# Optimization experiments

Hardware: AMD Instinct MI355X
Metric: run time of the kernel (lower is better)

Reference implementation:

```python
import jax, jax.numpy as jnp
import numpy as np

B, S, E, H = 2, 4096, 512, 8
DK = E // H


def setup_inputs() -> dict:
    k = jax.random.key(0)
    ks = jax.random.split(k, 11)
    sc = 0.02
    return {
        "query": jax.random.normal(ks[0], (B, S, E), jnp.float32),
        "key_in": jax.random.normal(ks[1], (B, S, E), jnp.float32),
        "value": jax.random.normal(ks[2], (B, S, E), jnp.float32),
        "Wq": jax.random.normal(ks[3], (E, E), jnp.float32) * sc,
        "bq": jax.random.normal(ks[4], (E,), jnp.float32) * sc,
        "Wk": jax.random.normal(ks[5], (E, E), jnp.float32) * sc,
        "bk": jax.random.normal(ks[6], (E,), jnp.float32) * sc,
        "Wv": jax.random.normal(ks[7], (E, E), jnp.float32) * sc,
        "bv": jax.random.normal(ks[8], (E,), jnp.float32) * sc,
        "Wo": jax.random.normal(ks[9], (E, E), jnp.float32) * sc,
        "bo": jax.random.normal(ks[10], (E,), jnp.float32) * sc,
    }


def reference(query, key_in, value, Wq, bq, Wk, bk, Wv, bv, Wo, bo):
    b, s, _ = query.shape
    # Linear projections
    q = query @ Wq + bq
    k = key_in @ Wk + bk
    v = value @ Wv + bv
    # [b, s, H, dk] -> [b, H, s, dk]
    q = q.reshape(b, s, H, DK).transpose(0, 2, 1, 3)
    k = k.reshape(b, s, H, DK).transpose(0, 2, 1, 3)
    v = v.reshape(b, s, H, DK).transpose(0, 2, 1, 3)
    # NOTE: source bug — softmax over UNSCALED scores (1/sqrt scaling in the
    # original is applied to a dead variable after softmax). Reproduce faithfully.
    scores = jnp.einsum("bhqd,bhkd->bhqk", q, k)  # [b,H,s,s] — O(N^2) materialized
    weights = jax.nn.softmax(scores.astype(jnp.float32), axis=-1)
    attn = jnp.einsum("bhqk,bhkd->bhqd", weights, v)
    # [b,H,s,dk] -> [b,s,E]
    concat = attn.transpose(0, 2, 1, 3).reshape(b, s, E)
    return concat @ Wo + bo
```

## Files before the change

kernel.cpp:

```cpp
#include <hip/hip_runtime.h>
#include <hip/hip_bf16.h>

#define B_  2
#define S_  4096
#define E_  512
#define H_  8
#define DK_ 64
#define M_  8192

typedef float f32x4  __attribute__((ext_vector_type(4)));
typedef float f32x16 __attribute__((ext_vector_type(16)));
typedef short s16x8  __attribute__((ext_vector_type(8)));
typedef short s16x4  __attribute__((ext_vector_type(4)));

static __device__ __forceinline__ short f2bf(float x) {
  __hip_bfloat16 h = __float2bfloat16(x);
  return __builtin_bit_cast(short, h);
}

static __device__ __forceinline__ f32x4 mfma32(s16x8 a, s16x8 b, f32x4 c) {
  return __builtin_amdgcn_mfma_f32_16x16x32_bf16(a, b, c, 0, 0, 0);
}

static __device__ __forceinline__ f32x16 mfma3232(s16x8 a, s16x8 b, f32x16 c) {
  return __builtin_amdgcn_mfma_f32_32x32x16_bf16(a, b, c, 0, 0, 0);
}

static __device__ __forceinline__ void gload_lds16(const void* g, void* l) {
  __builtin_amdgcn_global_load_lds(
      (const __attribute__((address_space(1))) unsigned int*)g,
      (__attribute__((address_space(3))) unsigned int*)l, 16, 0, 0);
}

static __device__ __forceinline__ int swz(int row, int colByte) {
  return row * 128 + (colByte ^ ((row & 7) << 4));
}

__global__ __launch_bounds__(256) void conv_bf16(const float* __restrict__ in,
                                                 short* __restrict__ out, int n4) {
  int i = blockIdx.x * 256 + threadIdx.x;
  if (i < n4) {
    float4 v = *((const float4*)in + i);
    s16x4 o;
    o[0] = f2bf(v.x); o[1] = f2bf(v.y); o[2] = f2bf(v.z); o[3] = f2bf(v.w);
    *((s16x4*)out + i) = o;
  }
}

__global__ __launch_bounds__(256) void conv_wT(const float* __restrict__ W,
                                               short* __restrict__ Wt) {
  int idx = blockIdx.x * 256 + threadIdx.x;
  int j = idx >> 9, k = idx & 511;
  Wt[idx] = f2bf(W[(size_t)k * E_ + j]);
}

static __device__ __forceinline__ void gemm_core_512(
    const short* __restrict__ A, const short* __restrict__ Bt,
    short* As, short* Bs, int tm, int tn, f32x4 acc[4][4]) {
  const int tid = threadIdx.x;
  const int wave = tid >> 6, lane = tid & 63;
  const int wm = (wave >> 1) * 64, wn = (wave & 1) * 64;
  const int c = lane & 15, g = lane >> 4;
  for (int kk = 0; kk < 512; kk += 64) {
#pragma unroll
    for (int i = 0; i < 4; ++i) {
      int ob = wave * 4096 + i * 1024 + lane * 16;
      int row = ob >> 7;
      int col = (ob & 127) >> 1;
      gload_lds16(A + (size_t)(tm + row) * 512 + kk + col,
                  (char*)As + wave * 4096 + i * 1024);
      gload_lds16(Bt + (size_t)(tn + row) * 512 + kk + col,
                  (char*)Bs + wave * 4096 + i * 1024);
    }
    __syncthreads();
#pragma unroll
    for (int s = 0; s < 2; ++s) {
      s16x8 af[4], bfr[4];
#pragma unroll
      for (int i = 0; i < 4; ++i)
        af[i] = *(const s16x8*)&As[(wm + i * 16 + c) * 64 + s * 32 + g * 8];
#pragma unroll
      for (int j = 0; j < 4; ++j)
        bfr[j] = *(const s16x8*)&Bs[(wn + j * 16 + c) * 64 + s * 32 + g * 8];
#pragma unroll
      for (int i = 0; i < 4; ++i)
#pragma unroll
        for (int j = 0; j < 4; ++j)
          acc[i][j] = mfma32(af[i], bfr[j], acc[i][j]);
    }
    __syncthreads();
  }
}

__global__ __launch_bounds__(256) void gemm_qkv(
    const short* __restrict__ Xq, const short* __restrict__ Xk,
    const short* __restrict__ Xv, const short* __restrict__ Wt,
    const float* __restrict__ bq, const float* __restrict__ bk,
    const float* __restrict__ bv,
    short* __restrict__ Qo, short* __restrict__ Ko, short* __restrict__ Vto) {
  __shared__ __align__(16) short As[128 * 64];
  __shared__ __align__(16) short Bs[128 * 64];
  const int z = blockIdx.z;
  const short* A = (z == 0) ? Xq : ((z == 1) ? Xk : Xv);
  const short* Bt = Wt + z * (E_ * E_);
  const float* bias = (z == 0) ? bq : ((z == 1) ? bk : bv);
  const int tm = blockIdx.x * 128, tn = blockIdx.y * 128;
  f32x4 acc[4][4] = {};
  gemm_core_512(A, Bt, As, Bs, tm, tn, acc);

  const int tid = threadIdx.x;
  const int wave = tid >> 6, lane = tid & 63;
  const int wm = (wave >> 1) * 64, wn = (wave & 1) * 64;
  const int c = lane & 15, g = lane >> 4;
#pragma unroll
  for (int i = 0; i < 4; ++i) {
#pragma unroll
    for (int j = 0; j < 4; ++j) {
      const int gc = tn + wn + j * 16 + c;
      const float bb = bias[gc];
      const int h = gc >> 6, dk = gc & 63;
#pragma unroll
      for (int r = 0; r < 4; ++r) {
        const int gr = tm + wm + i * 16 + g * 4 + r;
        const int b = gr >> 12, s = gr & 4095;
        const short hv = f2bf(acc[i][j][r] + bb);
        if (z == 2)
          Vto[(size_t)((b * H_ + h) * DK_ + dk) * S_ + s] = hv;
        else if (z == 1)
          Ko[(size_t)((b * H_ + h) * S_ + s) * DK_ + dk] = hv;
        else
          Qo[(size_t)((b * H_ + h) * S_ + s) * DK_ + dk] = hv;
      }
    }
  }
}

__global__ __launch_bounds__(256) void gemm_out(
    const short* __restrict__ AO, const short* __restrict__ Wot,
    const float* __restrict__ bo, float* __restrict__ out) {
  __shared__ __align__(16) short As[128 * 64];
  __shared__ __align__(16) short Bs[128 * 64];
  const int tm = blockIdx.x * 128, tn = blockIdx.y * 128;
  f32x4 acc[4][4] = {};
  gemm_core_512(AO, Wot, As, Bs, tm, tn, acc);

  const int tid = threadIdx.x;
  const int wave = tid >> 6, lane = tid & 63;
  const int wm = (wave >> 1) * 64, wn = (wave & 1) * 64;
  const int c = lane & 15, g = lane >> 4;
#pragma unroll
  for (int i = 0; i < 4; ++i) {
#pragma unroll
    for (int j = 0; j < 4; ++j) {
      const int gc = tn + wn + j * 16 + c;
      const float bb = bo[gc];
#pragma unroll
      for (int r = 0; r < 4; ++r) {
        const int gr = tm + wm + i * 16 + g * 4 + r;
        out[(size_t)gr * E_ + gc] = acc[i][j][r] + bb;
      }
    }
  }
}

__global__ __launch_bounds__(256, 2) void attn_fwd(
    const short* __restrict__ Q, const short* __restrict__ K,
    const short* __restrict__ Vt, short* __restrict__ O) {
  __shared__ __align__(16) short Ks[2][64 * 64];
  __shared__ __align__(16) short Vs[4][64 * 64];
  const int tid = threadIdx.x;
  const int wave = tid >> 6, lane = tid & 63;
  const int qi = lane & 31, hi = lane >> 5;
  const int bh = blockIdx.y;
  const int b = bh >> 3, h = bh & 7;
  const int q0 = blockIdx.x * 128 + wave * 32;
  const short* Qp = Q + (size_t)bh * S_ * DK_;
  const short* Kp = K + (size_t)bh * S_ * DK_;
  const short* Vp = Vt + (size_t)bh * DK_ * S_;

  s16x8 qf[4];
#pragma unroll
  for (int s = 0; s < 4; ++s)
    qf[s] = *(const s16x8*)(Qp + (size_t)(q0 + qi) * DK_ + s * 16 + hi * 8);

  f32x16 o0 = {}, o1 = {};
  f32x16 lacc = {};
  s16x8 ones;
#pragma unroll
  for (int e = 0; e < 8; ++e) ones[e] = (short)0x3F80;

  auto stageK = [&](int kt, int buf) {
#pragma unroll
    for (int r = 0; r < 2; ++r) {
      const int ob = wave * 2048 + r * 1024 + (lane << 4);
      const int row = ob >> 7;
      const int cbl = (ob & 127) ^ ((row & 7) << 4);
      const int srow = (row & 32) | ((row & 8) << 1) | ((row & 4) << 1) |
                       ((row & 16) >> 2) | (row & 3);
      gload_lds16(Kp + (size_t)(kt * 64 + srow) * DK_ + (cbl >> 1),
                  (char*)Ks[buf] + wave * 2048 + r * 1024);
    }
  };
  auto stageV = [&](int kt, int buf) {
#pragma unroll
    for (int r = 0; r < 2; ++r) {
      const int ob = wave * 2048 + r * 1024 + (lane << 4);
      const int row = ob >> 7;
      const int cbl = (ob & 127) ^ ((row & 7) << 4);
      gload_lds16(Vp + (size_t)row * S_ + kt * 64 + (cbl >> 1),
                  (char*)Vs[buf] + wave * 2048 + r * 1024);
    }
  };

  auto qk = [&](const short* Kbuf, f32x16& s0, f32x16& s1) {
    const char* Kc = (const char*)Kbuf;
    f32x16 t0 = {}, t1 = {};
#pragma unroll
    for (int s = 0; s < 4; ++s) {
      s16x8 ka = *(const s16x8*)(Kc + swz(qi, s * 32 + hi * 16));
      s16x8 kb = *(const s16x8*)(Kc + swz(32 + qi, s * 32 + hi * 16));
      t0 = mfma3232(ka, qf[s], t0);
      t1 = mfma3232(kb, qf[s], t1);
    }
    s0 = t0; s1 = t1;
  };

  auto softpv = [&](const f32x16& s0, const f32x16& s1, const short* Vbuf) {
    const char* Vc = (const char*)Vbuf;
    float p0[16], p1[16];
#pragma unroll
    for (int r = 0; r < 16; ++r) { p0[r] = __expf(s0[r]); p1[r] = __expf(s1[r]); }
    s16x8 pb[2][2];
#pragma unroll
    for (int ks = 0; ks < 2; ++ks)
#pragma unroll
      for (int j = 0; j < 8; ++j) {
        const int r = (j & 3) | (ks << 2) | ((j >> 2) << 3);
        pb[0][ks][j] = f2bf(p0[r]);
        pb[1][ks][j] = f2bf(p1[r]);
      }
    __builtin_amdgcn_s_setprio(1);
#pragma unroll
    for (int half = 0; half < 2; ++half)
#pragma unroll
      for (int ks = 0; ks < 2; ++ks) {
        s16x8 va0 = *(const s16x8*)(Vc + swz(qi, half * 64 + ks * 32 + hi * 16));
        s16x8 va1 = *(const s16x8*)(Vc + swz(32 + qi, half * 64 + ks * 32 + hi * 16));
        o0 = mfma3232(va0, pb[half][ks], o0);
        o1 = mfma3232(va1, pb[half][ks], o1);
        lacc = mfma3232(ones, pb[half][ks], lacc);
      }
    __builtin_amdgcn_s_setprio(0);
  };

  const int NT = S_ / 64;
  f32x16 sA0, sA1, sB0, sB1;

  stageK(0, 0); stageV(0, 0);
  __syncthreads();
  stageK(1, 1); stageV(1, 1);
  qk(Ks[0], sA0, sA1);
  __syncthreads();

  for (int t = 0; t < NT; t += 2) {
    if (t + 2 < NT) { stageK(t + 2, t & 1); stageV(t + 2, (t + 2) & 3); }
    qk(Ks[(t + 1) & 1], sB0, sB1);
    softpv(sA0, sA1, Vs[t & 3]);
    __syncthreads();
    if (t + 3 < NT) { stageK(t + 3, (t + 1) & 1); stageV(t + 3, (t + 3) & 3); }
    if (t + 2 < NT) qk(Ks[(t + 2) & 1], sA0, sA1);
    softpv(sB0, sB1, Vs[(t + 1) & 3]);
    __syncthreads();
  }

  const float rl = 1.f / lacc[0];
  short* Op = O + ((size_t)(b * S_ + q0 + qi)) * E_ + h * DK_;
#pragma unroll
  for (int rr = 0; rr < 4; ++rr) {
    s16x4 ov0, ov1;
#pragma unroll
    for (int e = 0; e < 4; ++e) {
      ov0[e] = f2bf(o0[rr * 4 + e] * rl);
      ov1[e] = f2bf(o1[rr * 4 + e] * rl);
    }
    *(s16x4*)(Op + rr * 8 + hi * 4) = ov0;
    *(s16x4*)(Op + 32 + rr * 8 + hi * 4) = ov1;
  }
}

extern "C" void kernel_launch(void* const* d_in, const int* in_sizes, int n_in,
                              void* d_out, int out_size, void* d_ws, size_t ws_size,
                              hipStream_t stream) {
  const float* query  = (const float*)d_in[0];
  const float* key_in = (const float*)d_in[1];
  const float* value  = (const float*)d_in[2];
  const float* Wq = (const float*)d_in[3];
  const float* bq = (const float*)d_in[4];
  const float* Wk = (const float*)d_in[5];
  const float* bk = (const float*)d_in[6];
  const float* Wv = (const float*)d_in[7];
  const float* bv = (const float*)d_in[8];
  const float* Wo = (const float*)d_in[9];
  const float* bo = (const float*)d_in[10];
  float* out = (float*)d_out;

  const size_t NA = (size_t)M_ * E_;
  short* ws  = (short*)d_ws;
  short* Xq  = ws;
  short* Xk  = Xq + NA;
  short* Xv  = Xk + NA;
  short* Wt  = Xv + NA;
  short* Wot = Wt + 3 * E_ * E_;
  short* Qb  = Wot + E_ * E_;
  short* Kb  = Qb + NA;
  short* Vtb = Kb + NA;
  short* AO  = Vtb + NA;

  conv_bf16<<<dim3(NA / 1024), 256, 0, stream>>>(query, Xq, (int)(NA / 4));
  conv_bf16<<<dim3(NA / 1024), 256, 0, stream>>>(key_in, Xk, (int)(NA / 4));
  conv_bf16<<<dim3(NA / 1024), 256, 0, stream>>>(value, Xv, (int)(NA / 4));
  conv_wT<<<dim3(E_ * E_ / 256), 256, 0, stream>>>(Wq, Wt);
  conv_wT<<<dim3(E_ * E_ / 256), 256, 0, stream>>>(Wk, Wt + E_ * E_);
  conv_wT<<<dim3(E_ * E_ / 256), 256, 0, stream>>>(Wv, Wt + 2 * E_ * E_);
  conv_wT<<<dim3(E_ * E_ / 256), 256, 0, stream>>>(Wo, Wot);

  gemm_qkv<<<dim3(M_ / 128, E_ / 128, 3), 256, 0, stream>>>(
      Xq, Xk, Xv, Wt, bq, bk, bv, Qb, Kb, Vtb);
  attn_fwd<<<dim3(S_ / 128, B_ * H_), 256, 0, stream>>>(Qb, Kb, Vtb, AO);
  gemm_out<<<dim3(M_ / 128, E_ / 128), 256, 0, stream>>>(AO, Wot, bo, out);
}
```

Baseline: 177.5 us.

## Merge conversion launches, fold log2e into Q, precompute attention LDS offsets

```diff
diff --git a/kernel.cpp b/kernel.cpp
--- a/kernel.cpp
+++ b/kernel.cpp
@@ -26,32 +26,44 @@
   return __builtin_amdgcn_mfma_f32_32x32x16_bf16(a, b, c, 0, 0, 0);
 }
 
+static __device__ __forceinline__ float fastexp2(float x) {
+#if __has_builtin(__builtin_amdgcn_exp2f)
+  return __builtin_amdgcn_exp2f(x);
+#else
+  return __expf(x * 0.69314718056f);
+#endif
+}
+
 static __device__ __forceinline__ void gload_lds16(const void* g, void* l) {
   __builtin_amdgcn_global_load_lds(
       (const __attribute__((address_space(1))) unsigned int*)g,
       (__attribute__((address_space(3))) unsigned int*)l, 16, 0, 0);
 }
 
-static __device__ __forceinline__ int swz(int row, int colByte) {
-  return row * 128 + (colByte ^ ((row & 7) << 4));
-}
-
-__global__ __launch_bounds__(256) void conv_bf16(const float* __restrict__ in,
-                                                 short* __restrict__ out, int n4) {
+__global__ __launch_bounds__(256) void conv_bf16_all(
+    const float* __restrict__ q, const float* __restrict__ k,
+    const float* __restrict__ v, short* __restrict__ out, int n4) {
+  const float* in = (blockIdx.y == 0) ? q : ((blockIdx.y == 1) ? k : v);
+  short* o = out + (size_t)blockIdx.y * (size_t)n4 * 4;
   int i = blockIdx.x * 256 + threadIdx.x;
   if (i < n4) {
-    float4 v = *((const float4*)in + i);
-    s16x4 o;
-    o[0] = f2bf(v.x); o[1] = f2bf(v.y); o[2] = f2bf(v.z); o[3] = f2bf(v.w);
-    *((s16x4*)out + i) = o;
-  }
-}
-
-__global__ __launch_bounds__(256) void conv_wT(const float* __restrict__ W,
-                                               short* __restrict__ Wt) {
+    float4 x = *((const float4*)in + i);
+    s16x4 r;
+    r[0] = f2bf(x.x); r[1] = f2bf(x.y); r[2] = f2bf(x.z); r[3] = f2bf(x.w);
+    *((s16x4*)o + i) = r;
+  }
+}
+
+__global__ __launch_bounds__(256) void conv_wT_all(
+    const float* __restrict__ Wq, const float* __restrict__ Wk,
+    const float* __restrict__ Wv, const float* __restrict__ Wo,
+    short* __restrict__ Wt) {
+  const float* W = (blockIdx.y == 0) ? Wq
+                   : ((blockIdx.y == 1) ? Wk : ((blockIdx.y == 2) ? Wv : Wo));
+  short* o = Wt + (size_t)blockIdx.y * (E_ * E_);
   int idx = blockIdx.x * 256 + threadIdx.x;
   int j = idx >> 9, k = idx & 511;
-  Wt[idx] = f2bf(W[(size_t)k * E_ + j]);
+  o[idx] = f2bf(W[(size_t)k * E_ + j]);
 }
 
 static __device__ __forceinline__ void gemm_core_512(
@@ -123,7 +135,9 @@
       for (int r = 0; r < 4; ++r) {
         const int gr = tm + wm + i * 16 + g * 4 + r;
         const int b = gr >> 12, s = gr & 4095;
-        const short hv = f2bf(acc[i][j][r] + bb);
+        float v = acc[i][j][r] + bb;
+        if (z == 0) v *= 1.44269504f;
+        const short hv = f2bf(v);
         if (z == 2)
           Vto[(size_t)((b * H_ + h) * DK_ + dk) * S_ + s] = hv;
         else if (z == 1)
@@ -189,47 +203,51 @@
 #pragma unroll
   for (int e = 0; e < 8; ++e) ones[e] = (short)0x3F80;
 
-  auto stageK = [&](int kt, int buf) {
+  int kOffL[2], vOffL[2];
+#pragma unroll
+  for (int r = 0; r < 2; ++r) {
+    const int j = wave * 2 + r;
+    const int row = (j >> 2) * 32 + qi;
+    const int srow = (row & 32) | ((row & 8) << 1) | ((row & 4) << 1) |
+                     ((row & 16) >> 2) | (row & 3);
+    kOffL[r] = srow * DK_ + (j & 3) * 16 + hi * 8;
+    vOffL[r] = ((j >> 2) * 32 + qi) * S_ + ((j >> 1) & 1) * 32 +
+               (j & 1) * 16 + hi * 8;
+  }
+
+  auto stage = [&](int kt) {
 #pragma unroll
     for (int r = 0; r < 2; ++r) {
-      const int ob = wave * 2048 + r * 1024 + (lane << 4);
-      const int row = ob >> 7;
-      const int cbl = (ob & 127) ^ ((row & 7) << 4);
-      const int srow = (row & 32) | ((row & 8) << 1) | ((row & 4) << 1) |
-                       ((row & 16) >> 2) | (row & 3);
-      gload_lds16(Kp + (size_t)(kt * 64 + srow) * DK_ + (cbl >> 1),
-                  (char*)Ks[buf] + wave * 2048 + r * 1024);
+      const int j = wave * 2 + r;
+      gload_lds16(Kp + (size_t)kt * 64 * DK_ + kOffL[r],
+                  (char*)Ks[kt & 1] + j * 1024);
+      gload_lds16(Vp + (size_t)kt * 64 + vOffL[r],
+                  (char*)Vs[kt & 3] + j * 1024);
     }
   };
-  auto stageV = [&](int kt, int buf) {
-#pragma unroll
-    for (int r = 0; r < 2; ++r) {
-      const int ob = wave * 2048 + r * 1024 + (lane << 4);
-      const int row = ob >> 7;
-      const int cbl = (ob & 127) ^ ((row & 7) << 4);
-      gload_lds16(Vp + (size_t)row * S_ + kt * 64 + (cbl >> 1),
-                  (char*)Vs[buf] + wave * 2048 + r * 1024);
-    }
-  };
+
+  const int lb = lane << 4;
 
   auto qk = [&](const short* Kbuf, f32x16& s0, f32x16& s1) {
-    const char* Kc = (const char*)Kbuf;
+    const char* Kc = (const char*)Kbuf + lb;
     f32x16 t0 = {}, t1 = {};
+    __builtin_amdgcn_s_setprio(1);
 #pragma unroll
     for (int s = 0; s < 4; ++s) {
-      s16x8 ka = *(const s16x8*)(Kc + swz(qi, s * 32 + hi * 16));
-      s16x8 kb = *(const s16x8*)(Kc + swz(32 + qi, s * 32 + hi * 16));
+      s16x8 ka = *(const s16x8*)(Kc + s * 1024);
+      s16x8 kb = *(const s16x8*)(Kc + 4096 + s * 1024);
       t0 = mfma3232(ka, qf[s], t0);
       t1 = mfma3232(kb, qf[s], t1);
     }
+    __builtin_amdgcn_s_setprio(0);
     s0 = t0; s1 = t1;
   };
 
   auto softpv = [&](const f32x16& s0, const f32x16& s1, const short* Vbuf) {
-    const char* Vc = (const char*)Vbuf;
+    const char* Vc = (const char*)Vbuf + lb;
     float p0[16], p1[16];
 #pragma unroll
-    for (int r = 0; r < 16; ++r) { p0[r] = __expf(s0[r]); p1[r] = __expf(s1[r]); }
+    for (int r = 0; r < 16; ++r) { p0[r] = fastexp2(s0[r]); p1[r] = fastexp2(s1[r]); }
     s16x8 pb[2][2];
 #pragma unroll
     for (int ks = 0; ks < 2; ++ks)
@@ -241,14 +259,14 @@
       }
     __builtin_amdgcn_s_setprio(1);
 #pragma unroll
-    for (int half = 0; half < 2; ++half)
+    for (int hf = 0; hf < 2; ++hf)
 #pragma unroll
       for (int ks = 0; ks < 2; ++ks) {
-        s16x8 va0 = *(const s16x8*)(Vc + swz(qi, half * 64 + ks * 32 + hi * 16));
-        s16x8 va1 = *(const s16x8*)(Vc + swz(32 + qi, half * 64 + ks * 32 + hi * 16));
-        o0 = mfma3232(va0, pb[half][ks], o0);
-        o1 = mfma3232(va1, pb[half][ks], o1);
-        lacc = mfma3232(ones, pb[half][ks], lacc);
+        s16x8 va0 = *(const s16x8*)(Vc + (hf * 2 + ks) * 1024);
+        s16x8 va1 = *(const s16x8*)(Vc + 4096 + (hf * 2 + ks) * 1024);
+        o0 = mfma3232(va0, pb[hf][ks], o0);
+        o1 = mfma3232(va1, pb[hf][ks], o1);
+        lacc = mfma3232(ones, pb[hf][ks], lacc);
       }
     __builtin_amdgcn_s_setprio(0);
   };
@@ -256,18 +274,18 @@
   const int NT = S_ / 64;
   f32x16 sA0, sA1, sB0, sB1;
 
-  stageK(0, 0); stageV(0, 0);
+  stage(0);
   __syncthreads();
-  stageK(1, 1); stageV(1, 1);
+  stage(1);
   qk(Ks[0], sA0, sA1);
   __syncthreads();
 
   for (int t = 0; t < NT; t += 2) {
-    if (t + 2 < NT) { stageK(t + 2, t & 1); stageV(t + 2, (t + 2) & 3); }
+    if (t + 2 < NT) stage(t + 2);
     qk(Ks[(t + 1) & 1], sB0, sB1);
     softpv(sA0, sA1, Vs[t & 3]);
     __syncthreads();
-    if (t + 3 < NT) { stageK(t + 3, (t + 1) & 1); stageV(t + 3, (t + 3) & 3); }
+    if (t + 3 < NT) stage(t + 3);
     if (t + 2 < NT) qk(Ks[(t + 2) & 1], sA0, sA1);
     softpv(sB0, sB1, Vs[(t + 1) & 3]);
     __syncthreads();
@@ -307,22 +325,18 @@
   const size_t NA = (size_t)M_ * E_;
   short* ws  = (short*)d_ws;
   short* Xq  = ws;
-  short* Xk  = Xq + NA;
-  short* Xv  = Xk + NA;
-  short* Wt  = Xv + NA;
+  short* Wt  = Xq + 3 * NA;
   short* Wot = Wt + 3 * E_ * E_;
-  short* Qb  = Wot + E_ * E_;
+  short* Qb  = Wt + 4 * E_ * E_;
   short* Kb  = Qb + NA;
   short* Vtb = Kb + NA;
   short* AO  = Vtb + NA;
-
-  conv_bf16<<<dim3(NA / 1024), 256, 0, stream>>>(query, Xq, (int)(NA / 4));
-  conv_bf16<<<dim3(NA / 1024), 256, 0, stream>>>(key_in, Xk, (int)(NA / 4));
-  conv_bf16<<<dim3(NA / 1024), 256, 0, stream>>>(value, Xv, (int)(NA / 4));
-  conv_wT<<<dim3(E_ * E_ / 256), 256, 0, stream>>>(Wq, Wt);
-  conv_wT<<<dim3(E_ * E_ / 256), 256, 0, stream>>>(Wk, Wt + E_ * E_);
-  conv_wT<<<dim3(E_ * E_ / 256), 256, 0, stream>>>(Wv, Wt + 2 * E_ * E_);
-  conv_wT<<<dim3(E_ * E_ / 256), 256, 0, stream>>>(Wo, Wot);
+  short* Xk  = Xq + NA;
+  short* Xv  = Xk + NA;
+
+  conv_bf16_all<<<dim3(NA / 1024, 3), 256, 0, stream>>>(
+      query, key_in, value, Xq, (int)(NA / 4));
+  conv_wT_all<<<dim3(E_ * E_ / 256, 4), 256, 0, stream>>>(Wq, Wk, Wv, Wo, Wt);
 
   gemm_qkv<<<dim3(M_ / 128, E_ / 128, 3), 256, 0, stream>>>(
       Xq, Xk, Xv, Wt, bq, bk, bv, Qb, Kb, Vtb);
```

After: 167.8 us. -5.5%, faster.
